# Optimization experiments

Measured on AMD Instinct MI355X. Metric: run time of the kernel, lower is better.

Reference implementation:

```python
import jax, jax.numpy as jnp
import numpy as np

TEMPERATURE = 1.0

def _cauchy_kernel(x, y, temperature):
    # pairwise squared distances via Gram trick: ||x_i - y_j||^2
    sq_x = jnp.sum(x * x, axis=1)  # [n]
    sq_y = jnp.sum(y * y, axis=1)  # [m]
    d2 = sq_x[:, None] + sq_y[None, :] - 2.0 * (x @ y.T)
    d2 = jnp.maximum(d2, 0.0)
    return 1.0 / (1.0 + d2 / temperature)


def setup_inputs() -> dict:
    key = jax.random.key(0)
    k1, k2 = jax.random.split(key)
    features = jax.random.normal(k1, (8192, 128), dtype=jnp.float32)
    labels = jax.random.randint(k2, (8192,), 0, 1000, dtype=jnp.int64)
    return {"features": features, "labels": labels}


def reference(features, labels):
    b = features.shape[0] // 2
    z1 = features[:b]
    z2 = features[b:]
    z11 = _cauchy_kernel(z1, z1, TEMPERATURE)  # [b,b]
    z22 = _cauchy_kernel(z2, z2, TEMPERATURE)  # [b,b]
    z12 = _cauchy_kernel(z1, z2, TEMPERATURE)  # [b,b]

    eye = jnp.eye(b, dtype=z11.dtype)
    # positive term: mean log of matched-pair kernel (diagonal of z12)
    pos = jnp.sum(jnp.log(jnp.diagonal(z12))) / b
    # negative terms: row sums over [z11 - I | z12] and [z12^T | z22 - I]
    n1 = jnp.mean(jnp.log((z11 - eye).sum(axis=1) + z12.sum(axis=1)))
    n2 = jnp.mean(jnp.log(z12.sum(axis=0) + (z22 - eye).sum(axis=1)))
    neg = (n1 + n2) / 2.0
    return -(pos - neg)
```

## Files before the change

### kernel.cpp

```cpp
#include <hip/hip_runtime.h>
#include <math.h>

#define N_TOTAL 8192
#define BHALF   4096
#define KDIM    128
#define NBLK    528

typedef __bf16 bf16x8 __attribute__((ext_vector_type(8)));
typedef __bf16 bf16x2 __attribute__((ext_vector_type(2)));
typedef float  f32x4  __attribute__((ext_vector_type(4)));

#define GLOAD_LDS16(GSRC, LDST)                                                \
    __builtin_amdgcn_global_load_lds(                                          \
        (const __attribute__((address_space(1))) void*)(GSRC),                 \
        (__attribute__((address_space(3))) void*)(LDST), 16, 0, 0)

__global__ __launch_bounds__(256) void k_prep_pos(const float* __restrict__ F,
                                                  __bf16* __restrict__ Fbf,
                                                  float* __restrict__ sq,
                                                  float* __restrict__ T,
                                                  float* __restrict__ posPart) {
    int t = threadIdx.x;
    int w = t >> 6, l = t & 63;
    int p = blockIdx.x * 4 + w;
    const float2* r1 = (const float2*)(F + (size_t)p * KDIM);
    const float2* r2 = (const float2*)(F + (size_t)(p + BHALF) * KDIM);
    float2 a = r1[l];
    float2 c = r2[l];

    float s1 = fmaf(a.x, a.x, a.y * a.y);
    float s2 = fmaf(c.x, c.x, c.y * c.y);
    float dp = fmaf(a.x, c.x, a.y * c.y);
#pragma unroll
    for (int off = 32; off > 0; off >>= 1) {
        s1 += __shfl_down(s1, off);
        s2 += __shfl_down(s2, off);
        dp += __shfl_down(dp, off);
    }

    bf16x2 pa, pc;
    pa[0] = (__bf16)a.x; pa[1] = (__bf16)a.y;
    pc[0] = (__bf16)c.x; pc[1] = (__bf16)c.y;
    ((bf16x2*)(Fbf + (size_t)p * KDIM))[l] = pa;
    ((bf16x2*)(Fbf + (size_t)(p + BHALF) * KDIM))[l] = pc;

    __shared__ float posRed[4];
    if (l == 0) {
        sq[p] = s1;
        sq[p + BHALF] = s2;
        T[p] = 0.0f;
        T[p + BHALF] = 0.0f;
        float d2 = fmaxf(s1 + s2 - 2.0f * dp, 0.0f);
        posRed[w] = logf(1.0f + d2);
    }
    __syncthreads();
    if (t == 0)
        posPart[blockIdx.x] = posRed[0] + posRed[1] + posRed[2] + posRed[3];
}

__global__ __launch_bounds__(512, 2) void k_pairwise(
        const __bf16* __restrict__ Fbf,
        const float* __restrict__ sq,
        float* __restrict__ T) {
    int b = blockIdx.x;
    int si = 0, cum = 0;
    while (cum + (32 - si) <= b) { cum += 32 - si; ++si; }
    int bl = b - cum;
    int cj0 = 2 * si + 2 * bl;
    int I0 = si * 256;
    bool masked = (bl == 0);

    __shared__ __align__(16) __bf16 As[256 * 128];
    __shared__ __align__(16) __bf16 Bs[2][128 * 128];
    __shared__ float rowAcc[256][2];
    __shared__ float colAcc[128][4];

    int t = threadIdx.x;
    int w = t >> 6;
    int l = t & 63;
    int wr = w >> 1, wc = w & 1;
    int low = l & 15, kb = l >> 4;

    const __bf16* FA = Fbf + (size_t)I0 * KDIM;
    const __bf16* FB0 = Fbf + (size_t)cj0 * 128 * KDIM;
#pragma unroll
    for (int it = 0; it < 8; ++it) {
        int f = it * 512 + t;
        int row = f >> 4;
        int sg = f & 15;
        int g = sg ^ (row & 15);
        GLOAD_LDS16(FA + row * KDIM + g * 8, As + (size_t)f * 8);
    }
#pragma unroll
    for (int it = 0; it < 4; ++it) {
        int f = it * 512 + t;
        int row = f >> 4;
        int sg = f & 15;
        int g = sg ^ (row & 15);
        GLOAD_LDS16(FB0 + row * KDIM + g * 8, Bs[0] + (size_t)f * 8);
    }
    __syncthreads();

    const bf16x8* Asg = (const bf16x8*)As;
    float rowPart[4][4] = {};

    float sqi[4][4];
#pragma unroll
    for (int fr = 0; fr < 4; ++fr)
#pragma unroll
        for (int r = 0; r < 4; ++r)
            sqi[fr][r] = sq[I0 + wr * 64 + fr * 16 + kb * 4 + r];

    for (int kt = 0; kt < 2; ++kt) {
        int tj = cj0 + kt;
        int J0 = tj * 128;

        if (kt == 0) {
            const __bf16* FB1 = Fbf + (size_t)(cj0 + 1) * 128 * KDIM;
#pragma unroll
            for (int it = 0; it < 4; ++it) {
                int f = it * 512 + t;
                int row = f >> 4;
                int sg = f & 15;
                int g = sg ^ (row & 15);
                GLOAD_LDS16(FB1 + row * KDIM + g * 8, Bs[1] + (size_t)f * 8);
            }
        }

        const bf16x8* Bsg = (const bf16x8*)Bs[kt];
        f32x4 acc[4][4] = {};
#pragma unroll
        for (int s = 0; s < 4; ++s) {
            int g = s * 4 + kb;
            bf16x8 aF[4], bF[4];
#pragma unroll
            for (int fr = 0; fr < 4; ++fr) {
                int R = wr * 64 + fr * 16 + low;
                aF[fr] = Asg[R * 16 + (g ^ low)];
            }
#pragma unroll
            for (int fc = 0; fc < 4; ++fc) {
                int C = wc * 64 + fc * 16 + low;
                bF[fc] = Bsg[C * 16 + (g ^ low)];
            }
#pragma unroll
            for (int fr = 0; fr < 4; ++fr)
#pragma unroll
                for (int fc = 0; fc < 4; ++fc)
                    acc[fr][fc] = __builtin_amdgcn_mfma_f32_16x16x32_bf16(
                        aF[fr], bF[fc], acc[fr][fc], 0, 0, 0);
        }

        float sqj[4];
#pragma unroll
        for (int fc = 0; fc < 4; ++fc)
            sqj[fc] = sq[J0 + wc * 64 + fc * 16 + low];

        float colPart[4] = {0.f, 0.f, 0.f, 0.f};
#define EPI(MASK)                                                              \
        _Pragma("unroll")                                                      \
        for (int fr = 0; fr < 4; ++fr) {                                       \
            _Pragma("unroll")                                                  \
            for (int fc = 0; fc < 4; ++fc) {                                   \
                _Pragma("unroll")                                              \
                for (int r = 0; r < 4; ++r) {                                  \
                    float d2 = sqi[fr][r] + sqj[fc] - 2.0f * acc[fr][fc][r];   \
                    d2 = fmaxf(d2, 0.0f);                                      \
                    float v = __builtin_amdgcn_rcpf(1.0f + d2);                \
                    if (MASK) {                                                \
                        int R = I0 + wr * 64 + fr * 16 + kb * 4 + r;           \
                        int C = J0 + wc * 64 + fc * 16 + low;                  \
                        v = (C > R) ? v : 0.0f;                                \
                    }                                                          \
                    rowPart[fr][r] += v;                                       \
                    colPart[fc] += v;                                          \
                }                                                              \
            }                                                                  \
        }
        if (masked) { EPI(true) } else { EPI(false) }
#undef EPI

#pragma unroll
        for (int fc = 0; fc < 4; ++fc) {
            float x = colPart[fc];
            x += __shfl_xor(x, 16);
            x += __shfl_xor(x, 32);
            if (kb == 0)
                colAcc[wc * 64 + fc * 16 + low][wr] = x;
        }
        __syncthreads();
        if (t < 128)
            atomicAdd(&T[J0 + t],
                      colAcc[t][0] + colAcc[t][1] + colAcc[t][2] + colAcc[t][3]);
        __syncthreads();
    }

#pragma unroll
    for (int fr = 0; fr < 4; ++fr)
#pragma unroll
        for (int r = 0; r < 4; ++r) {
            float x = rowPart[fr][r];
            x += __shfl_xor(x, 1);
            x += __shfl_xor(x, 2);
            x += __shfl_xor(x, 4);
            x += __shfl_xor(x, 8);
            if (low == 0)
                rowAcc[wr * 64 + fr * 16 + kb * 4 + r][wc] = x;
        }
    __syncthreads();
    if (t < 256)
        atomicAdd(&T[I0 + t], rowAcc[t][0] + rowAcc[t][1]);
}

__global__ __launch_bounds__(512) void k_final(const float* __restrict__ T,
                                               const float* __restrict__ posPart,
                                               float* __restrict__ out) {
    int t = threadIdx.x;
    float s = 0.0f;
    for (int i = t; i < N_TOTAL; i += 512) s += logf(T[i]);
    s *= 0.5f;
    for (int i = t; i < 1024; i += 512) s += posPart[i];
#pragma unroll
    for (int off = 32; off > 0; off >>= 1) s += __shfl_down(s, off);
    __shared__ float red[8];
    int w = t >> 6, l = t & 63;
    if (l == 0) red[w] = s;
    __syncthreads();
    if (t == 0) {
        float S = 0.0f;
#pragma unroll
        for (int i = 0; i < 8; ++i) S += red[i];
        out[0] = S / (float)BHALF;
    }
}

extern "C" void kernel_launch(void* const* d_in, const int* in_sizes, int n_in,
                              void* d_out, int out_size, void* d_ws, size_t ws_size,
                              hipStream_t stream) {
    const float* F = (const float*)d_in[0];
    float* out = (float*)d_out;

    char* ws = (char*)d_ws;
    __bf16* Fbf     = (__bf16*)ws;
    float*  sq      = (float*)(ws + (size_t)N_TOTAL * KDIM * 2);
    float*  T       = sq + N_TOTAL;
    float*  posPart = T + N_TOTAL;

    k_prep_pos<<<BHALF / 4, 256, 0, stream>>>(F, Fbf, sq, T, posPart);
    k_pairwise<<<NBLK, 512, 0, stream>>>(Fbf, sq, T);
    k_final<<<1, 512, 0, stream>>>(T, posPart, out);
}
```

Baseline: 98.61 us.

## Use 128x128 triangular tiles with direct global fragment loads in pairwise kernel

Replaces the 256-row strip blocks, each covering two 128-column tiles staged through LDS, with one 256-thread block per 128x128 upper-triangular tile. The block index is mapped to a tile pair with a closed-form square-root formula plus correction loops. MFMA fragments are now read straight from global memory instead of async LDS staging, and row and column sums are flushed once per block. The intent is better load balance across CUs from many more, smaller blocks and less LDS and sync overhead, at the cost of more L2 traffic and uncoalesced fragment reads.

```diff
diff --git a/kernel.cpp b/kernel.cpp
--- a/kernel.cpp
+++ b/kernel.cpp
@@ -4,16 +4,12 @@
 #define N_TOTAL 8192
 #define BHALF   4096
 #define KDIM    128
-#define NBLK    528
+#define NTILES  64
+#define NBLK    (NTILES * (NTILES + 1) / 2)
 
 typedef __bf16 bf16x8 __attribute__((ext_vector_type(8)));
 typedef __bf16 bf16x2 __attribute__((ext_vector_type(2)));
 typedef float  f32x4  __attribute__((ext_vector_type(4)));
-
-#define GLOAD_LDS16(GSRC, LDST)                                                \
-    __builtin_amdgcn_global_load_lds(                                          \
-        (const __attribute__((address_space(1))) void*)(GSRC),                 \
-        (__attribute__((address_space(3))) void*)(LDST), 16, 0, 0)
 
 __global__ __launch_bounds__(256) void k_prep_pos(const float* __restrict__ F,
                                                   __bf16* __restrict__ Fbf,
@@ -58,22 +54,20 @@
         posPart[blockIdx.x] = posRed[0] + posRed[1] + posRed[2] + posRed[3];
 }
 
-__global__ __launch_bounds__(512, 2) void k_pairwise(
+__global__ __launch_bounds__(256, 3) void k_pairwise(
         const __bf16* __restrict__ Fbf,
         const float* __restrict__ sq,
         float* __restrict__ T) {
     int b = blockIdx.x;
-    int si = 0, cum = 0;
-    while (cum + (32 - si) <= b) { cum += 32 - si; ++si; }
-    int bl = b - cum;
-    int cj0 = 2 * si + 2 * bl;
-    int I0 = si * 256;
-    bool masked = (bl == 0);
-
-    __shared__ __align__(16) __bf16 As[256 * 128];
-    __shared__ __align__(16) __bf16 Bs[2][128 * 128];
-    __shared__ float rowAcc[256][2];
-    __shared__ float colAcc[128][4];
+    int ti = (int)floorf((129.0f - sqrtf(16641.0f - 8.0f * (float)b)) * 0.5f);
+    while (ti * (129 - ti) / 2 > b) --ti;
+    while ((ti + 1) * (128 - ti) / 2 <= b) ++ti;
+    int tj = ti + (b - ti * (129 - ti) / 2);
+    int I = ti * 128, J = tj * 128;
+    bool diag = (ti == tj);
+
+    __shared__ float rowAcc[128][2];
+    __shared__ float colAcc[128][2];
 
     int t = threadIdx.x;
     int w = t >> 6;
@@ -81,119 +75,61 @@
     int wr = w >> 1, wc = w & 1;
     int low = l & 15, kb = l >> 4;
 
-    const __bf16* FA = Fbf + (size_t)I0 * KDIM;
-    const __bf16* FB0 = Fbf + (size_t)cj0 * 128 * KDIM;
-#pragma unroll
-    for (int it = 0; it < 8; ++it) {
-        int f = it * 512 + t;
-        int row = f >> 4;
-        int sg = f & 15;
-        int g = sg ^ (row & 15);
-        GLOAD_LDS16(FA + row * KDIM + g * 8, As + (size_t)f * 8);
-    }
-#pragma unroll
-    for (int it = 0; it < 4; ++it) {
-        int f = it * 512 + t;
-        int row = f >> 4;
-        int sg = f & 15;
-        int g = sg ^ (row & 15);
-        GLOAD_LDS16(FB0 + row * KDIM + g * 8, Bs[0] + (size_t)f * 8);
-    }
-    __syncthreads();
-
-    const bf16x8* Asg = (const bf16x8*)As;
+    const bf16x8* Fg = (const bf16x8*)Fbf;
+
+    f32x4 acc[4][4] = {};
+#pragma unroll
+    for (int s = 0; s < 4; ++s) {
+        int g = s * 4 + kb;
+        bf16x8 aF[4], bF[4];
+#pragma unroll
+        for (int fr = 0; fr < 4; ++fr)
+            aF[fr] = Fg[(size_t)(I + wr * 64 + fr * 16 + low) * 16 + g];
+#pragma unroll
+        for (int fc = 0; fc < 4; ++fc)
+            bF[fc] = Fg[(size_t)(J + wc * 64 + fc * 16 + low) * 16 + g];
+#pragma unroll
+        for (int fr = 0; fr < 4; ++fr)
+#pragma unroll
+            for (int fc = 0; fc < 4; ++fc)
+                acc[fr][fc] = __builtin_amdgcn_mfma_f32_16x16x32_bf16(
+                    aF[fr], bF[fc], acc[fr][fc], 0, 0, 0);
+    }
+
+    float sqi[4][4], sqj[4];
+#pragma unroll
+    for (int fr = 0; fr < 4; ++fr)
+#pragma unroll
+        for (int r = 0; r < 4; ++r)
+            sqi[fr][r] = sq[I + wr * 64 + fr * 16 + kb * 4 + r];
+#pragma unroll
+    for (int fc = 0; fc < 4; ++fc)
+        sqj[fc] = sq[J + wc * 64 + fc * 16 + low];
+
     float rowPart[4][4] = {};
-
-    float sqi[4][4];
-#pragma unroll
-    for (int fr = 0; fr < 4; ++fr)
-#pragma unroll
-        for (int r = 0; r < 4; ++r)
-            sqi[fr][r] = sq[I0 + wr * 64 + fr * 16 + kb * 4 + r];
-
-    for (int kt = 0; kt < 2; ++kt) {
-        int tj = cj0 + kt;
-        int J0 = tj * 128;
-
-        if (kt == 0) {
-            const __bf16* FB1 = Fbf + (size_t)(cj0 + 1) * 128 * KDIM;
-#pragma unroll
-            for (int it = 0; it < 4; ++it) {
-                int f = it * 512 + t;
-                int row = f >> 4;
-                int sg = f & 15;
-                int g = sg ^ (row & 15);
-                GLOAD_LDS16(FB1 + row * KDIM + g * 8, Bs[1] + (size_t)f * 8);
-            }
-        }
-
-        const bf16x8* Bsg = (const bf16x8*)Bs[kt];
-        f32x4 acc[4][4] = {};
-#pragma unroll
-        for (int s = 0; s < 4; ++s) {
-            int g = s * 4 + kb;
-            bf16x8 aF[4], bF[4];
-#pragma unroll
-            for (int fr = 0; fr < 4; ++fr) {
-                int R = wr * 64 + fr * 16 + low;
-                aF[fr] = Asg[R * 16 + (g ^ low)];
-            }
-#pragma unroll
-            for (int fc = 0; fc < 4; ++fc) {
-                int C = wc * 64 + fc * 16 + low;
-                bF[fc] = Bsg[C * 16 + (g ^ low)];
-            }
-#pragma unroll
-            for (int fr = 0; fr < 4; ++fr)
-#pragma unroll
-                for (int fc = 0; fc < 4; ++fc)
-                    acc[fr][fc] = __builtin_amdgcn_mfma_f32_16x16x32_bf16(
-                        aF[fr], bF[fc], acc[fr][fc], 0, 0, 0);
-        }
-
-        float sqj[4];
-#pragma unroll
-        for (int fc = 0; fc < 4; ++fc)
-            sqj[fc] = sq[J0 + wc * 64 + fc * 16 + low];
-
-        float colPart[4] = {0.f, 0.f, 0.f, 0.f};
+    float colPart[4] = {0.f, 0.f, 0.f, 0.f};
 #define EPI(MASK)                                                              \
+    _Pragma("unroll")                                                          \
+    for (int fr = 0; fr < 4; ++fr) {                                           \
         _Pragma("unroll")                                                      \
-        for (int fr = 0; fr < 4; ++fr) {                                       \
+        for (int fc = 0; fc < 4; ++fc) {                                       \
             _Pragma("unroll")                                                  \
-            for (int fc = 0; fc < 4; ++fc) {                                   \
-                _Pragma("unroll")                                              \
-                for (int r = 0; r < 4; ++r) {                                  \
-                    float d2 = sqi[fr][r] + sqj[fc] - 2.0f * acc[fr][fc][r];   \
-                    d2 = fmaxf(d2, 0.0f);                                      \
-                    float v = __builtin_amdgcn_rcpf(1.0f + d2);                \
-                    if (MASK) {                                                \
-                        int R = I0 + wr * 64 + fr * 16 + kb * 4 + r;           \
-                        int C = J0 + wc * 64 + fc * 16 + low;                  \
-                        v = (C > R) ? v : 0.0f;                                \
-                    }                                                          \
-                    rowPart[fr][r] += v;                                       \
-                    colPart[fc] += v;                                          \
+            for (int r = 0; r < 4; ++r) {                                      \
+                float d2 = sqi[fr][r] + sqj[fc] - 2.0f * acc[fr][fc][r];       \
+                d2 = fmaxf(d2, 0.0f);                                          \
+                float v = __builtin_amdgcn_rcpf(1.0f + d2);                    \
+                if (MASK) {                                                    \
+                    int R = wr * 64 + fr * 16 + kb * 4 + r;                    \
+                    int C = wc * 64 + fc * 16 + low;                           \
+                    v = (C > R) ? v : 0.0f;     \
                 }                                                              \
+                rowPart[fr][r] += v;                                           \
+                colPart[fc] += v;                                              \
             }                                                                  \
-        }
-        if (masked) { EPI(true) } else { EPI(false) }
+        }                                                                      \
+    }
+    if (diag) { EPI(true) } else { EPI(false) }
 #undef EPI
-
-#pragma unroll
-        for (int fc = 0; fc < 4; ++fc) {
-            float x = colPart[fc];
-            x += __shfl_xor(x, 16);
-            x += __shfl_xor(x, 32);
-            if (kb == 0)
-                colAcc[wc * 64 + fc * 16 + low][wr] = x;
-        }
-        __syncthreads();
-        if (t < 128)
-            atomicAdd(&T[J0 + t],
-                      colAcc[t][0] + colAcc[t][1] + colAcc[t][2] + colAcc[t][3]);
-        __syncthreads();
-    }
 
 #pragma unroll
     for (int fr = 0; fr < 4; ++fr)
@@ -207,9 +143,23 @@
             if (low == 0)
                 rowAcc[wr * 64 + fr * 16 + kb * 4 + r][wc] = x;
         }
+
+#pragma unroll
+    for (int fc = 0; fc < 4; ++fc) {
+        float x = colPart[fc];
+        x += __shfl_xor(x, 16);
+        x += __shfl_xor(x, 32);
+        if (kb == 0)
+            colAcc[wc * 64 + fc * 16 + low][wr] = x;
+    }
     __syncthreads();
-    if (t < 256)
-        atomicAdd(&T[I0 + t], rowAcc[t][0] + rowAcc[t][1]);
+
+    if (t < 128) {
+        atomicAdd(&T[I + t], rowAcc[t][0] + rowAcc[t][1]);
+    } else {
+        int c = t - 128;
+        atomicAdd(&T[J + c], colAcc[c][0] + colAcc[c][1]);
+    }
 }
 
 __global__ __launch_bounds__(512) void k_final(const float* __restrict__ T,
@@ -247,6 +197,6 @@
     float*  posPart = T + N_TOTAL;
 
     k_prep_pos<<<BHALF / 4, 256, 0, stream>>>(F, Fbf, sq, T, posPart);
-    k_pairwise<<<NBLK, 512, 0, stream>>>(Fbf, sq, T);
+    k_pairwise<<<NBLK, 256, 0, stream>>>(Fbf, sq, T);
     k_final<<<1, 512, 0, stream>>>(T, posPart, out);
 }
```

After: 103.8 us. 5.2% more time.
